# Kernel tuning notes

Measured on AMD Instinct MI355X. Metric: run time of the kernel, lower is better.

The kernel has to match this reference:

```python
import jax, jax.numpy as jnp
import numpy as np

B, S, D, H = 8, 1024, 1024, 16
DH = D // H


def setup_inputs() -> dict:
    key = jax.random.key(0)
    ks = jax.random.split(key, 7)
    scale = 1.0 / np.sqrt(DH)
    return {
        "sequences": jax.random.normal(ks[0], (B, S, D), dtype=jnp.float32),
        "Wq": jax.random.uniform(ks[1], (H, DH, DH), jnp.float32, -scale, scale),
        "bq": jax.random.uniform(ks[2], (H, DH), jnp.float32, -scale, scale),
        "Wk": jax.random.uniform(ks[3], (H, DH, DH), jnp.float32, -scale, scale),
        "bk": jax.random.uniform(ks[4], (H, DH), jnp.float32, -scale, scale),
        "Wv": jax.random.uniform(ks[5], (H, DH, DH), jnp.float32, -scale, scale),
        "bv": jax.random.uniform(ks[6], (H, DH), jnp.float32, -scale, scale),
    }


def reference(sequences, Wq, bq, Wk, bk, Wv, bv):
    # split channels into heads: [B,S,H,DH]
    x = sequences.reshape(B, S, H, DH)
    # per-head linear maps (torch Linear: y = x @ W.T + b)
    q = jnp.einsum("bshd,hed->bshe", x, Wq) + bq  # [B,S,H,DH]
    k = jnp.einsum("bshd,hed->bshe", x, Wk) + bk
    v = jnp.einsum("bshd,hed->bshe", x, Wv) + bv
    scores = jnp.einsum("bshd,bthd->bhst", q, k) / jnp.sqrt(jnp.asarray(DH, x.dtype))
    attn = jax.nn.softmax(scores, axis=-1)  # [B,H,S,S]
    out = jnp.einsum("bhst,bthd->bshd", attn, v)  # [B,S,H,DH]
    return out.reshape(B, S, D)
```

## Files before the change

kernel.cpp:

```cpp
#include <hip/hip_runtime.h>
#include <hip/hip_bf16.h>


constexpr int NB = 8, NS = 1024, ND = 1024, NH = 16, NDH = 64;

typedef __bf16 bf16x8 __attribute__((ext_vector_type(8)));
typedef float f32x4 __attribute__((ext_vector_type(4)));

__device__ __forceinline__ f32x4 mfma16(bf16x8 a, bf16x8 b, f32x4 c) {
  return __builtin_amdgcn_mfma_f32_16x16x32_bf16(a, b, c, 0, 0, 0);
}

__device__ __forceinline__ float fast_exp2(float x) {
#if __has_builtin(__builtin_amdgcn_exp2f)
  return __builtin_amdgcn_exp2f(x);
#else
  return __builtin_exp2f(x);
#endif
}

__device__ __forceinline__ unsigned pack2(float lo, float hi) {
  unsigned uh = __builtin_bit_cast(unsigned, hi) + 0x8000u;
  unsigned ul = __builtin_bit_cast(unsigned, lo) + 0x8000u;
  return __builtin_amdgcn_perm(uh, ul, 0x07060302u);
}

__device__ __forceinline__ unsigned pack2t(float lo, float hi) {
  return __builtin_amdgcn_perm(__builtin_bit_cast(unsigned, hi),
                               __builtin_bit_cast(unsigned, lo), 0x07060302u);
}

__device__ __forceinline__ bf16x8 cvt2bf8(float4 lo, float4 hi) {
  bf16x8 r;
  r[0] = (__bf16)lo.x; r[1] = (__bf16)lo.y; r[2] = (__bf16)lo.z; r[3] = (__bf16)lo.w;
  r[4] = (__bf16)hi.x; r[5] = (__bf16)hi.y; r[6] = (__bf16)hi.z; r[7] = (__bf16)hi.w;
  return r;
}

__device__ __forceinline__ void gload16(const __hip_bfloat16* g, __hip_bfloat16* l) {
  __builtin_amdgcn_global_load_lds(
      (const __attribute__((address_space(1))) void*)g,
      (__attribute__((address_space(3))) void*)l, 16, 0, 0);
}

__global__ __launch_bounds__(256) void qkv_proj_kernel(
    const float* __restrict__ x,
    const float* __restrict__ Wq, const float* __restrict__ bq,
    const float* __restrict__ Wk, const float* __restrict__ bk,
    const float* __restrict__ Wv, const float* __restrict__ bv,
    __hip_bfloat16* __restrict__ Qo, __hip_bfloat16* __restrict__ Ko,
    __hip_bfloat16* __restrict__ Vt) {
  __shared__ __align__(16) __hip_bfloat16 Wlds[3][NDH][72];
  const int tid = threadIdx.x;
  const int wave = tid >> 6, lane = tid & 63;
  const int m = lane & 15, quad = lane >> 4;
  const int h = blockIdx.x & (NH - 1);
  const int sblk = blockIdx.x >> 4;

  const float* Ws[3] = {Wq + h * 4096, Wk + h * 4096, Wv + h * 4096};
#pragma unroll
  for (int mt = 0; mt < 3; mt++) {
#pragma unroll
    for (int p = 0; p < 4; p++) {
      int idx = (p * 256 + tid) * 4;
      float4 v = *(const float4*)(Ws[mt] + idx);
      uint2 w;
      w.x = pack2(v.x, v.y);
      w.y = pack2(v.z, v.w);
      *(uint2*)&Wlds[mt][idx >> 6][idx & 63] = w;
    }
  }
  __syncthreads();

  float bq4[4][4], bk4[4][4], bvv[4];
#pragma unroll
  for (int nt = 0; nt < 4; nt++) {
    float4 a = *(const float4*)(bq + h * 64 + nt * 16 + quad * 4);
    float4 c = *(const float4*)(bk + h * 64 + nt * 16 + quad * 4);
    bq4[nt][0] = a.x; bq4[nt][1] = a.y; bq4[nt][2] = a.z; bq4[nt][3] = a.w;
    bk4[nt][0] = c.x; bk4[nt][1] = c.y; bk4[nt][2] = c.z; bk4[nt][3] = c.w;
    bvv[nt] = bv[h * 64 + nt * 16 + m];
  }

  const int rowbase = sblk * 256 + wave * 64;
  bf16x8 Xf[4][2];
#pragma unroll
  for (int st = 0; st < 4; st++) {
    const float* xp = x + (size_t)(rowbase + st * 16 + m) * ND + h * NDH + quad * 8;
#pragma unroll
    for (int c = 0; c < 2; c++) {
      float4 lo = *(const float4*)(xp + c * 32);
      float4 hi = *(const float4*)(xp + c * 32 + 4);
      Xf[st][c] = cvt2bf8(lo, hi);
    }
  }

  const int b = rowbase >> 10;
  const int s0 = rowbase & 1023;
  const float qscale = 0.18033688011112042f;

#pragma unroll
  for (int mt = 0; mt < 3; mt++) {
#pragma unroll
    for (int nt = 0; nt < 4; nt++) {
      bf16x8 w0 = *(const bf16x8*)&Wlds[mt][nt * 16 + m][quad * 8];
      bf16x8 w1 = *(const bf16x8*)&Wlds[mt][nt * 16 + m][32 + quad * 8];
#pragma unroll
      for (int st = 0; st < 4; st++) {
        f32x4 acc = {0.f, 0.f, 0.f, 0.f};
        if (mt < 2) {
          acc = mfma16(w0, Xf[st][0], acc);
          acc = mfma16(w1, Xf[st][1], acc);
          const int srow = s0 + st * 16 + m;
          uint2 w;
          if (mt == 0) {
            w.x = pack2((acc[0] + bq4[nt][0]) * qscale, (acc[1] + bq4[nt][1]) * qscale);
            w.y = pack2((acc[2] + bq4[nt][2]) * qscale, (acc[3] + bq4[nt][3]) * qscale);
            *(uint2*)(Qo + ((size_t)(b * NH + h) * NS + srow) * NDH +
                      nt * 16 + quad * 4) = w;
          } else {
            w.x = pack2(acc[0] + bk4[nt][0], acc[1] + bk4[nt][1]);
            w.y = pack2(acc[2] + bk4[nt][2], acc[3] + bk4[nt][3]);
            *(uint2*)(Ko + ((size_t)(b * NH + h) * NS + srow) * NDH +
                      nt * 16 + quad * 4) = w;
          }
        } else {
          acc = mfma16(Xf[st][0], w0, acc);
          acc = mfma16(Xf[st][1], w1, acc);
          uint2 w;
          w.x = pack2(acc[0] + bvv[nt], acc[1] + bvv[nt]);
          w.y = pack2(acc[2] + bvv[nt], acc[3] + bvv[nt]);
          *(uint2*)(Vt + ((size_t)(b * NH + h) * NDH + nt * 16 + m) * NS + s0 +
                    st * 16 + quad * 4) = w;
        }
      }
    }
  }
}

__global__ __launch_bounds__(256, 4) void attn_kernel(
    const __hip_bfloat16* __restrict__ Q,
    const __hip_bfloat16* __restrict__ K,
    const __hip_bfloat16* __restrict__ Vt,
    float* __restrict__ out) {
  __shared__ __align__(16) __hip_bfloat16 Kt[2][64][64];
  __shared__ __align__(16) __hip_bfloat16 Vl[2][64][64];

  const int tid = threadIdx.x;
  const int wave = tid >> 6, lane = tid & 63;
  const int m = lane & 15, quad = lane >> 4;

  const int xcd = blockIdx.x & 7;
  const int j = blockIdx.x >> 3;
  const int bh = xcd * 16 + (j & 15);
  const int qblk = j >> 4;
  const int qbase = qblk * 128 + wave * 32;

  const __hip_bfloat16* Qp = Q + (size_t)bh * NS * NDH;
  const __hip_bfloat16* Kp = K + (size_t)bh * NS * NDH;
  const __hip_bfloat16* Vp = Vt + (size_t)bh * NDH * NS;

  bf16x8 Bq[2][2];
#pragma unroll
  for (int g = 0; g < 2; g++)
#pragma unroll
    for (int dh = 0; dh < 2; dh++)
      Bq[g][dh] = *(const bf16x8*)(Qp + (size_t)(qbase + g * 16 + m) * NDH +
                                   dh * 32 + quad * 8);

  f32x4 accO[2][4];
  f32x4 lsum[2];
#pragma unroll
  for (int g = 0; g < 2; g++) {
    lsum[g] = (f32x4){0.f, 0.f, 0.f, 0.f};
#pragma unroll
    for (int nt = 0; nt < 4; nt++) accO[g][nt] = (f32x4){0.f, 0.f, 0.f, 0.f};
  }
  bf16x8 ones8;
#pragma unroll
  for (int i = 0; i < 8; i++) ones8[i] = (__bf16)1.0f;
  const f32x4 fzero = {0.f, 0.f, 0.f, 0.f};

  const int krow = 8 * (m >> 2) + (m & 3);
  const int fK = (m & 3) ^ (((m >> 2) & 1) << 2);
  const int kc0 = (quad ^ fK) * 8;
  const int vbase = quad ^ (m & 7);

#define STAGE(buf, tb)                                                        \
  {                                                                           \
    _Pragma("unroll") for (int l = 0; l < 2; l++) {                           \
      const int krb = wave * 16 + l * 8;                                      \
      const int csK = (lane & 7) ^ ((lane >> 3) & 3) ^ (l << 2);              \
      gload16(Kp + (size_t)((tb) * 64 + krb + (lane >> 3)) * NDH + csK * 8,   \
              &Kt[buf][krb][0]);                                              \
      const int vrb = wave * 16 + l * 8;                                      \
      const int csV = (lane & 7) ^ (lane >> 3);                               \
      gload16(Vp + (size_t)(vrb + (lane >> 3)) * NS + (tb) * 64 + csV * 8,    \
              &Vl[buf][vrb][0]);                                              \
    }                                                                         \
  }

  STAGE(0, 0);

  for (int tb = 0; tb < 16; tb++) {
    const int cur = tb & 1;
    __syncthreads();
    if (tb + 1 < 16) STAGE(cur ^ 1, tb + 1);

    bf16x8 Pa0[2], Pa1[2];
    {
      uint4 u[2];
#pragma unroll
      for (int p = 0; p < 2; p++) {
        const __hip_bfloat16* kr = &Kt[cur][4 * p + krow][0];
        bf16x8 k0 = *(const bf16x8*)(kr + kc0);
        bf16x8 k1 = *(const bf16x8*)(kr + (kc0 ^ 32));
#pragma unroll
        for (int g = 0; g < 2; g++) {
          f32x4 a = mfma16(k1, Bq[g][1], mfma16(k0, Bq[g][0], fzero));
          unsigned w0 = pack2t(fast_exp2(a[0]), fast_exp2(a[1]));
          unsigned w1 = pack2t(fast_exp2(a[2]), fast_exp2(a[3]));
          if (p == 0) { u[g].x = w0; u[g].y = w1; }
          else        { u[g].z = w0; u[g].w = w1; }
        }
      }
#pragma unroll
      for (int g = 0; g < 2; g++) Pa0[g] = __builtin_bit_cast(bf16x8, u[g]);
    }

    f32x4 a1[2][2];
#pragma unroll
    for (int p = 0; p < 2; p++) {
      const __hip_bfloat16* kr = &Kt[cur][32 + 4 * p + krow][0];
      bf16x8 k0 = *(const bf16x8*)(kr + kc0);
      bf16x8 k1 = *(const bf16x8*)(kr + (kc0 ^ 32));
#pragma unroll
      for (int g = 0; g < 2; g++)
        a1[p][g] = mfma16(k1, Bq[g][1], mfma16(k0, Bq[g][0], fzero));
    }

#pragma unroll
    for (int g = 0; g < 2; g++) lsum[g] = mfma16(Pa0[g], ones8, lsum[g]);
#pragma unroll
    for (int nt = 0; nt < 4; nt++) {
      const int off0 = vbase << 3;
      bf16x8 v = *(const bf16x8*)&Vl[cur][nt * 16 + m][off0];
#pragma unroll
      for (int g = 0; g < 2; g++)
        accO[g][nt] = mfma16(Pa0[g], v, accO[g][nt]);
    }

    {
      uint4 u[2];
#pragma unroll
      for (int p = 0; p < 2; p++)
#pragma unroll
        for (int g = 0; g < 2; g++) {
          unsigned w0 = pack2t(fast_exp2(a1[p][g][0]), fast_exp2(a1[p][g][1]));
          unsigned w1 = pack2t(fast_exp2(a1[p][g][2]), fast_exp2(a1[p][g][3]));
          if (p == 0) { u[g].x = w0; u[g].y = w1; }
          else        { u[g].z = w0; u[g].w = w1; }
        }
#pragma unroll
      for (int g = 0; g < 2; g++) Pa1[g] = __builtin_bit_cast(bf16x8, u[g]);
    }

#pragma unroll
    for (int g = 0; g < 2; g++) lsum[g] = mfma16(Pa1[g], ones8, lsum[g]);
#pragma unroll
    for (int nt = 0; nt < 4; nt++) {
      const int off1 = (vbase ^ 4) << 3;
      bf16x8 v = *(const bf16x8*)&Vl[cur][nt * 16 + m][off1];
#pragma unroll
      for (int g = 0; g < 2; g++)
        accO[g][nt] = mfma16(Pa1[g], v, accO[g][nt]);
    }
  }
#undef STAGE

  const int b = bh >> 4, h = bh & (NH - 1);
#pragma unroll
  for (int g = 0; g < 2; g++) {
#pragma unroll
    for (int r = 0; r < 4; r++) {
      float inv = 1.0f / lsum[g][r];
      int srow = qbase + g * 16 + quad * 4 + r;
      float* op = out + (size_t)(b * NS + srow) * ND + h * NDH;
#pragma unroll
      for (int nt = 0; nt < 4; nt++) op[nt * 16 + m] = accO[g][nt][r] * inv;
    }
  }
}

extern "C" void kernel_launch(void* const* d_in, const int* in_sizes, int n_in,
                              void* d_out, int out_size, void* d_ws, size_t ws_size,
                              hipStream_t stream) {
  const float* x  = (const float*)d_in[0];
  const float* Wq = (const float*)d_in[1];
  const float* bq = (const float*)d_in[2];
  const float* Wk = (const float*)d_in[3];
  const float* bk = (const float*)d_in[4];
  const float* Wv = (const float*)d_in[5];
  const float* bv = (const float*)d_in[6];
  float* out = (float*)d_out;

  const size_t elems = (size_t)NB * NH * NS * NDH;
  __hip_bfloat16* Qw = (__hip_bfloat16*)d_ws;
  __hip_bfloat16* Kw = Qw + elems;
  __hip_bfloat16* Vw = Kw + elems;

  qkv_proj_kernel<<<512, 256, 0, stream>>>(x, Wq, bq, Wk, bk, Wv, bv, Qw, Kw, Vw);
  attn_kernel<<<1024, 256, 0, stream>>>(Qw, Kw, Vw, out);
}
```

Baseline: 141.5 us.

## Drop LDS weight staging in QKV projection and double grid size

```diff
diff --git a/kernel.cpp b/kernel.cpp
--- a/kernel.cpp
+++ b/kernel.cpp
@@ -43,34 +43,30 @@
       (__attribute__((address_space(3))) void*)l, 16, 0, 0);
 }
 
-__global__ __launch_bounds__(256) void qkv_proj_kernel(
+__global__ __launch_bounds__(256, 4) void qkv_proj_kernel(
     const float* __restrict__ x,
     const float* __restrict__ Wq, const float* __restrict__ bq,
     const float* __restrict__ Wk, const float* __restrict__ bk,
     const float* __restrict__ Wv, const float* __restrict__ bv,
     __hip_bfloat16* __restrict__ Qo, __hip_bfloat16* __restrict__ Ko,
     __hip_bfloat16* __restrict__ Vt) {
-  __shared__ __align__(16) __hip_bfloat16 Wlds[3][NDH][72];
   const int tid = threadIdx.x;
   const int wave = tid >> 6, lane = tid & 63;
   const int m = lane & 15, quad = lane >> 4;
   const int h = blockIdx.x & (NH - 1);
   const int sblk = blockIdx.x >> 4;
-
-  const float* Ws[3] = {Wq + h * 4096, Wk + h * 4096, Wv + h * 4096};
-#pragma unroll
-  for (int mt = 0; mt < 3; mt++) {
-#pragma unroll
-    for (int p = 0; p < 4; p++) {
-      int idx = (p * 256 + tid) * 4;
-      float4 v = *(const float4*)(Ws[mt] + idx);
-      uint2 w;
-      w.x = pack2(v.x, v.y);
-      w.y = pack2(v.z, v.w);
-      *(uint2*)&Wlds[mt][idx >> 6][idx & 63] = w;
-    }
-  }
-  __syncthreads();
+  const int rowbase = sblk * 128 + wave * 32;
+
+  float4 xr[2][2][2];
+#pragma unroll
+  for (int st = 0; st < 2; st++) {
+    const float* xp = x + (size_t)(rowbase + st * 16 + m) * ND + h * NDH + quad * 8;
+#pragma unroll
+    for (int c = 0; c < 2; c++) {
+      xr[st][c][0] = *(const float4*)(xp + c * 32);
+      xr[st][c][1] = *(const float4*)(xp + c * 32 + 4);
+    }
+  }
 
   float bq4[4][4], bk4[4][4], bvv[4];
 #pragma unroll
@@ -82,31 +78,30 @@
     bvv[nt] = bv[h * 64 + nt * 16 + m];
   }
 
-  const int rowbase = sblk * 256 + wave * 64;
-  bf16x8 Xf[4][2];
-#pragma unroll
-  for (int st = 0; st < 4; st++) {
-    const float* xp = x + (size_t)(rowbase + st * 16 + m) * ND + h * NDH + quad * 8;
-#pragma unroll
-    for (int c = 0; c < 2; c++) {
-      float4 lo = *(const float4*)(xp + c * 32);
-      float4 hi = *(const float4*)(xp + c * 32 + 4);
-      Xf[st][c] = cvt2bf8(lo, hi);
-    }
-  }
+  bf16x8 Xf[2][2];
+#pragma unroll
+  for (int st = 0; st < 2; st++)
+#pragma unroll
+    for (int c = 0; c < 2; c++) Xf[st][c] = cvt2bf8(xr[st][c][0], xr[st][c][1]);
 
   const int b = rowbase >> 10;
   const int s0 = rowbase & 1023;
   const float qscale = 0.18033688011112042f;
+  const float* Ws[3] = {Wq + h * 4096, Wk + h * 4096, Wv + h * 4096};
 
 #pragma unroll
   for (int mt = 0; mt < 3; mt++) {
-#pragma unroll
+#pragma unroll 2
     for (int nt = 0; nt < 4; nt++) {
-      bf16x8 w0 = *(const bf16x8*)&Wlds[mt][nt * 16 + m][quad * 8];
-      bf16x8 w1 = *(const bf16x8*)&Wlds[mt][nt * 16 + m][32 + quad * 8];
-#pragma unroll
-      for (int st = 0; st < 4; st++) {
+      const float* wp = Ws[mt] + (nt * 16 + m) * 64;
+      float4 a0 = *(const float4*)(wp + quad * 8);
+      float4 a1 = *(const float4*)(wp + quad * 8 + 4);
+      float4 b0 = *(const float4*)(wp + 32 + quad * 8);
+      float4 b1 = *(const float4*)(wp + 32 + quad * 8 + 4);
+      bf16x8 w0 = cvt2bf8(a0, a1);
+      bf16x8 w1 = cvt2bf8(b0, b1);
+#pragma unroll
+      for (int st = 0; st < 2; st++) {
         f32x4 acc = {0.f, 0.f, 0.f, 0.f};
         if (mt < 2) {
           acc = mfma16(w0, Xf[st][0], acc);
@@ -309,6 +304,6 @@
   __hip_bfloat16* Kw = Qw + elems;
   __hip_bfloat16* Vw = Kw + elems;
 
-  qkv_proj_kernel<<<512, 256, 0, stream>>>(x, Wq, bq, Wk, bk, Wv, bv, Qw, Kw, Vw);
+  qkv_proj_kernel<<<1024, 256, 0, stream>>>(x, Wq, bq, Wk, bk, Wv, bv, Qw, Kw, Vw);
   attn_kernel<<<1024, 256, 0, stream>>>(Qw, Kw, Vw, out);
 }
```

Result: slower. 153.3 us (+8.4%).
